# Optimization experiments

Measured on AMD Instinct MI355X. Metric: run time of the kernel, lower is better.

## Reference

```python
import jax, jax.numpy as jnp
import numpy as np

N = 4_194_304  # rays
D = 8          # depth values per ray
IGNORE_VALUE = 0.0  # config.multiDepthIgnoreValue[net_idx]


def setup_inputs() -> dict:
    key = jax.random.key(0)
    k1, k2 = jax.random.split(key)
    outputs = jax.random.normal(k1, (N, D), dtype=jnp.float32)
    targets = jax.random.uniform(k2, (N, D), dtype=jnp.float32)
    return {"outputs": outputs, "targets": targets}


def reference(outputs, targets):
    n, d = outputs.shape
    rows = jnp.arange(n)
    big = jnp.finfo(outputs.dtype).max

    # Sequential greedy matching: for each target column i, find the closest
    # remaining output per row, record its index, and knock it out with +inf.
    def step(out_cpy, t_col):
        # out_cpy: [N, D], t_col: [N]
        ids = jnp.argmin(jnp.abs(out_cpy - t_col[:, None]), axis=-1)  # [N]
        out_cpy = out_cpy.at[rows, ids].set(big)
        return out_cpy, ids

    _, ids_all = jax.lax.scan(step, outputs, targets.T)  # ids_all: [D, N]
    resort_indices = ids_all.T  # [N, D]

    outputs_shfled = jnp.take_along_axis(outputs, resort_indices, axis=1)
    # targets.data / outputs_shfled.data -> stop_gradient semantics for seltargets
    seltargets = jnp.where(targets != IGNORE_VALUE, targets,
                           jax.lax.stop_gradient(outputs_shfled))
    return jnp.mean((outputs_shfled - seltargets) ** 2)
```

## Files before the change

### kernel.cpp

```cpp
#include <hip/hip_runtime.h>
#include <cfloat>


#define DVALS 8
#define ROWS_PER_THREAD 4

__global__ __launch_bounds__(256) void mdmse_match_kernel(
    const float* __restrict__ outputs,
    const float* __restrict__ targets,
    float* __restrict__ out,
    int n_rows,
    float inv_count)
{
    int tid = blockIdx.x * blockDim.x + threadIdx.x;
    int stride = gridDim.x * blockDim.x;

    float local = 0.0f;

    for (int base = tid; base < n_rows; base += stride * ROWS_PER_THREAD) {
        float4 ov[ROWS_PER_THREAD][2];
        float4 tv4[ROWS_PER_THREAD][2];
        bool valid[ROWS_PER_THREAD];
#pragma unroll
        for (int k = 0; k < ROWS_PER_THREAD; ++k) {
            int r = base + k * stride;
            valid[k] = (r < n_rows);
            if (valid[k]) {
                const float4* op = reinterpret_cast<const float4*>(outputs + (size_t)r * DVALS);
                const float4* tp = reinterpret_cast<const float4*>(targets + (size_t)r * DVALS);
                ov[k][0] = op[0]; ov[k][1] = op[1];
                tv4[k][0] = tp[0]; tv4[k][1] = tp[1];
            }
        }

#pragma unroll
        for (int k = 0; k < ROWS_PER_THREAD; ++k) {
            if (!valid[k]) continue;
            float cpy[DVALS] = {ov[k][0].x, ov[k][0].y, ov[k][0].z, ov[k][0].w,
                                ov[k][1].x, ov[k][1].y, ov[k][1].z, ov[k][1].w};
            float t[DVALS]   = {tv4[k][0].x, tv4[k][0].y, tv4[k][0].z, tv4[k][0].w,
                                tv4[k][1].x, tv4[k][1].y, tv4[k][1].z, tv4[k][1].w};

#pragma unroll
            for (int i = 0; i < DVALS; ++i) {
                float tc = t[i];
                float bd = FLT_MAX;
                int bi = -1;
#pragma unroll
                for (int j = 0; j < DVALS; ++j) {
                    float d = fabsf(cpy[j] - tc);
                    bool better = d < bd;
                    bd = better ? d : bd;
                    bi = better ? j : bi;
                }
#pragma unroll
                for (int j = 0; j < DVALS; ++j)
                    cpy[j] = (bi == j) ? FLT_MAX : cpy[j];

                float c = (tc != 0.0f) ? bd : 0.0f;
                local = fmaf(c, c, local);
            }
        }
    }

#pragma unroll
    for (int off = 32; off > 0; off >>= 1)
        local += __shfl_down(local, off, 64);

    __shared__ float wsum[4];
    int lane = threadIdx.x & 63;
    int wid  = threadIdx.x >> 6;
    if (lane == 0) wsum[wid] = local;
    __syncthreads();

    if (threadIdx.x == 0) {
        float s = wsum[0] + wsum[1] + wsum[2] + wsum[3];
        atomicAdd(out, s * inv_count);
    }
}

extern "C" void kernel_launch(void* const* d_in, const int* in_sizes, int n_in,
                              void* d_out, int out_size, void* d_ws, size_t ws_size,
                              hipStream_t stream)
{
    const float* outputs = (const float*)d_in[0];
    const float* targets = (const float*)d_in[1];
    float* out = (float*)d_out;

    const int n_rows = in_sizes[0] / DVALS;

    hipMemsetAsync(out, 0, sizeof(float), stream);

    const int block = 256;
    long long want = ((long long)n_rows + block * ROWS_PER_THREAD - 1) /
                     (block * ROWS_PER_THREAD);
    int grid = (int)want;
    if (grid < 1) grid = 1;

    const float inv_count = 1.0f / ((float)n_rows * (float)DVALS);
    mdmse_match_kernel<<<grid, block, 0, stream>>>(outputs, targets, out,
                                                   n_rows, inv_count);
}
```

Before: 280.8 us.

## Pack distance and index into uint keys for branchless min-tree argmin

Replaces the sequential compare-select argmin with a packed integer key: the absolute difference's bits with the low three mantissa bits replaced by the column index, reduced by a balanced unsigned-min tree. It also interleaves the four rows per thread across the depth loop for ILP, uses clamped loads with a weight instead of per-row branches, and adds a sched barrier and launch bounds occupancy hint. The packing truncates the distance's low mantissa bits, so ties and near-ties may resolve differently and the loss is slightly approximated.

```diff
diff --git a/kernel.cpp b/kernel.cpp
--- a/kernel.cpp
+++ b/kernel.cpp
@@ -1,66 +1,73 @@
 #include <hip/hip_runtime.h>
 #include <cfloat>
+#include <stdint.h>
 
 
 #define DVALS 8
-#define ROWS_PER_THREAD 4
+#define RPT 4
 
-__global__ __launch_bounds__(256) void mdmse_match_kernel(
+__device__ __forceinline__ uint32_t umin2(uint32_t a, uint32_t b) {
+    return a < b ? a : b;
+}
+
+__global__ __launch_bounds__(256, 4) void mdmse_match_kernel(
     const float* __restrict__ outputs,
     const float* __restrict__ targets,
     float* __restrict__ out,
     int n_rows,
     float inv_count)
 {
-    int tid = blockIdx.x * blockDim.x + threadIdx.x;
-    int stride = gridDim.x * blockDim.x;
+    const int tid = blockIdx.x * blockDim.x + threadIdx.x;
+    const int stride = gridDim.x * blockDim.x;
 
     float local = 0.0f;
 
-    for (int base = tid; base < n_rows; base += stride * ROWS_PER_THREAD) {
-        float4 ov[ROWS_PER_THREAD][2];
-        float4 tv4[ROWS_PER_THREAD][2];
-        bool valid[ROWS_PER_THREAD];
+    for (int base = tid; base < n_rows; base += stride * RPT) {
+        float cpy[RPT][DVALS];
+        float t[RPT][DVALS];
+        float w[RPT];
+
 #pragma unroll
-        for (int k = 0; k < ROWS_PER_THREAD; ++k) {
+        for (int k = 0; k < RPT; ++k) {
             int r = base + k * stride;
-            valid[k] = (r < n_rows);
-            if (valid[k]) {
-                const float4* op = reinterpret_cast<const float4*>(outputs + (size_t)r * DVALS);
-                const float4* tp = reinterpret_cast<const float4*>(targets + (size_t)r * DVALS);
-                ov[k][0] = op[0]; ov[k][1] = op[1];
-                tv4[k][0] = tp[0]; tv4[k][1] = tp[1];
+            w[k] = (r < n_rows) ? 1.0f : 0.0f;
+            int rc = (r < n_rows) ? r : (n_rows - 1);
+            const float4* op = reinterpret_cast<const float4*>(outputs + (size_t)rc * DVALS);
+            const float4* tp = reinterpret_cast<const float4*>(targets + (size_t)rc * DVALS);
+            float4 o0 = op[0], o1 = op[1];
+            float4 t0 = tp[0], t1 = tp[1];
+            cpy[k][0]=o0.x; cpy[k][1]=o0.y; cpy[k][2]=o0.z; cpy[k][3]=o0.w;
+            cpy[k][4]=o1.x; cpy[k][5]=o1.y; cpy[k][6]=o1.z; cpy[k][7]=o1.w;
+            t[k][0]=t0.x; t[k][1]=t0.y; t[k][2]=t0.z; t[k][3]=t0.w;
+            t[k][4]=t1.x; t[k][5]=t1.y; t[k][6]=t1.z; t[k][7]=t1.w;
+        }
+        __builtin_amdgcn_sched_barrier(0);
+
+        float rs[RPT] = {0.0f, 0.0f, 0.0f, 0.0f};
+#pragma unroll
+        for (int i = 0; i < DVALS; ++i) {
+#pragma unroll
+            for (int k = 0; k < RPT; ++k) {
+                float tc = t[k][i];
+                uint32_t dp[DVALS];
+#pragma unroll
+                for (int j = 0; j < DVALS; ++j) {
+                    float diff = cpy[k][j] - tc;
+                    dp[j] = (__float_as_uint(diff) & 0x7FFFFFF8u) | (uint32_t)j;
+                }
+                uint32_t best = umin2(umin2(umin2(dp[0], dp[1]), umin2(dp[2], dp[3])),
+                                      umin2(umin2(dp[4], dp[5]), umin2(dp[6], dp[7])));
+#pragma unroll
+                for (int j = 0; j < DVALS; ++j)
+                    cpy[k][j] = (dp[j] == best) ? FLT_MAX : cpy[k][j];
+                float bd = __uint_as_float(best & 0xFFFFFFF8u);
+                float c = (tc != 0.0f) ? bd : 0.0f;
+                rs[k] = fmaf(c, c, rs[k]);
             }
         }
-
 #pragma unroll
-        for (int k = 0; k < ROWS_PER_THREAD; ++k) {
-            if (!valid[k]) continue;
-            float cpy[DVALS] = {ov[k][0].x, ov[k][0].y, ov[k][0].z, ov[k][0].w,
-                                ov[k][1].x, ov[k][1].y, ov[k][1].z, ov[k][1].w};
-            float t[DVALS]   = {tv4[k][0].x, tv4[k][0].y, tv4[k][0].z, tv4[k][0].w,
-                                tv4[k][1].x, tv4[k][1].y, tv4[k][1].z, tv4[k][1].w};
-
-#pragma unroll
-            for (int i = 0; i < DVALS; ++i) {
-                float tc = t[i];
-                float bd = FLT_MAX;
-                int bi = -1;
-#pragma unroll
-                for (int j = 0; j < DVALS; ++j) {
-                    float d = fabsf(cpy[j] - tc);
-                    bool better = d < bd;
-                    bd = better ? d : bd;
-                    bi = better ? j : bi;
-                }
-#pragma unroll
-                for (int j = 0; j < DVALS; ++j)
-                    cpy[j] = (bi == j) ? FLT_MAX : cpy[j];
-
-                float c = (tc != 0.0f) ? bd : 0.0f;
-                local = fmaf(c, c, local);
-            }
-        }
+        for (int k = 0; k < RPT; ++k)
+            local = fmaf(w[k], rs[k], local);
     }
 
 #pragma unroll
@@ -92,8 +99,8 @@
     hipMemsetAsync(out, 0, sizeof(float), stream);
 
     const int block = 256;
-    long long want = ((long long)n_rows + block * ROWS_PER_THREAD - 1) /
-                     (block * ROWS_PER_THREAD);
+    long long want = ((long long)n_rows + (long long)block * RPT - 1) /
+                     ((long long)block * RPT);
     int grid = (int)want;
     if (grid < 1) grid = 1;
 
```

After: 283.5 us. No clear change (+1.0%).
